# Optimization experiments

Measured on AMD Instinct MI355X. Metric: run time of the kernel, lower is better.

Reference implementation:

```python
import jax, jax.numpy as jnp
import numpy as np

D_MODEL = 2048
N_HEADS = 16
N_KV_HEADS = 4
HEAD_DIM = D_MODEL // N_HEADS  # 128
ROPE_BASE = 10000.0


def _rope_tables(T, head_dim):
    half = head_dim // 2
    theta = 1.0 / (ROPE_BASE ** (jnp.arange(half, dtype=jnp.float32) / half))
    m = jnp.arange(T, dtype=jnp.float32)
    freqs = jnp.outer(m, theta)  # (T, half)
    return jnp.cos(freqs), jnp.sin(freqs)


def _apply_rope(x, cos, sin):
    # x: (B, H, T, hd); rotate first/second halves as pairs
    half = x.shape[-1] // 2
    x1, x2 = x[..., :half], x[..., half:]
    cos = cos[None, None, :, :]
    sin = sin[None, None, :, :]
    return jnp.concatenate([x1 * cos - x2 * sin, x1 * sin + x2 * cos], axis=-1)


def setup_inputs() -> dict:
    key = jax.random.key(0)
    ks = jax.random.split(key, 5)
    B, T = 4, 2048
    x = jax.random.normal(ks[0], (B, T, D_MODEL), dtype=jnp.float32)
    Wq = jax.random.normal(ks[1], (D_MODEL, N_HEADS * HEAD_DIM), dtype=jnp.float32) * 0.02
    Wk = jax.random.normal(ks[2], (D_MODEL, N_KV_HEADS * HEAD_DIM), dtype=jnp.float32) * 0.02
    Wv = jax.random.normal(ks[3], (D_MODEL, N_KV_HEADS * HEAD_DIM), dtype=jnp.float32) * 0.02
    Wo = jax.random.normal(ks[4], (N_HEADS * HEAD_DIM, D_MODEL), dtype=jnp.float32) * (0.02 / np.sqrt(2.0))
    return {"x": x, "Wq": Wq, "Wk": Wk, "Wv": Wv, "Wo": Wo}


def reference(x, Wq, Wk, Wv, Wo):
    B, T, C = x.shape
    groups = N_HEADS // N_KV_HEADS

    # QKV projections
    q = (x @ Wq).reshape(B, T, N_HEADS, HEAD_DIM).transpose(0, 2, 1, 3)      # (B,H,T,hd)
    k = (x @ Wk).reshape(B, T, N_KV_HEADS, HEAD_DIM).transpose(0, 2, 1, 3)   # (B,Hkv,T,hd)
    v = (x @ Wv).reshape(B, T, N_KV_HEADS, HEAD_DIM).transpose(0, 2, 1, 3)

    # RoPE on q and k
    cos, sin = _rope_tables(T, HEAD_DIM)
    q = _apply_rope(q, cos, sin)
    k = _apply_rope(k, cos, sin)

    # GQA: repeat each kv head `groups` times
    k = jnp.repeat(k, groups, axis=1)  # (B,H,T,hd)
    v = jnp.repeat(v, groups, axis=1)

    # Attention scores with ALiBi bias and causal mask
    scale = 1.0 / np.sqrt(HEAD_DIM)
    scores = jnp.einsum('bhqd,bhkd->bhqk', q, k) * scale  # (B,H,T,T)

    pos = jnp.arange(T)
    dist = jnp.minimum(pos[None, :] - pos[:, None], 0).astype(jnp.float32)  # (T,T), <=0
    slopes = 2.0 ** (-8.0 * jnp.arange(1, N_HEADS + 1, dtype=jnp.float32) / N_HEADS)
    alibi = slopes[:, None, None] * dist[None, :, :]  # (H,T,T)
    scores = scores + alibi[None]

    causal = pos[None, :] > pos[:, None]  # True = future = blocked
    scores = jnp.where(causal[None, None], -jnp.inf, scores)

    weights = jax.nn.softmax(scores, axis=-1)
    out = jnp.einsum('bhqk,bhkd->bhqd', weights, v)  # (B,H,T,hd)
    out = out.transpose(0, 2, 1, 3).reshape(B, T, N_HEADS * HEAD_DIM)
    return out @ Wo
```

## Files before the change

kernel.cpp:

```cpp
#include <hip/hip_runtime.h>
#include <hip/hip_bf16.h>
#include <stdint.h>

#define T_SEQ 2048
#define DM    2048
#define NH    16
#define NKVH  4
#define HD    128
#define NBATCH 4
#define BT    (NBATCH * T_SEQ)
#define ATT_SCALE 0.08838834764831845f
#define LOG2E 1.4426950408889634f

typedef __attribute__((ext_vector_type(8))) short bf16x8;
typedef __attribute__((ext_vector_type(4))) float f32x4;
typedef __attribute__((ext_vector_type(16))) float f32x16;
typedef __attribute__((ext_vector_type(8))) unsigned short ushort8;
typedef __attribute__((ext_vector_type(4))) unsigned short ushort4v;

static __device__ __forceinline__ unsigned short f2bf(float f) {
  __hip_bfloat16 h = __float2bfloat16(f);
  return __builtin_bit_cast(unsigned short, h);
}
static __device__ __forceinline__ float bf2f(unsigned short u) {
  unsigned int v = ((unsigned int)u) << 16;
  return __builtin_bit_cast(float, v);
}
static __device__ __forceinline__ unsigned int packbf2(float a, float b) {
  return (unsigned int)f2bf(a) | ((unsigned int)f2bf(b) << 16);
}

#define GLDS16(g, l)                                                        \
  __builtin_amdgcn_global_load_lds(                                         \
      (const __attribute__((address_space(1))) void*)(g),                   \
      (__attribute__((address_space(3))) void*)(l), 16, 0, 0)

__global__ __launch_bounds__(256) void castx_k(const float* __restrict__ x,
                                               unsigned short* __restrict__ xb) {
  int i = (blockIdx.x * 256 + threadIdx.x) * 4;
  float4 v = *(const float4*)&x[i];
  ushort4v o;
  o[0] = f2bf(v.x); o[1] = f2bf(v.y); o[2] = f2bf(v.z); o[3] = f2bf(v.w);
  *(ushort4v*)&xb[i] = o;
}

__global__ __launch_bounds__(256) void transw_k(const float* __restrict__ src,
                                                unsigned short* __restrict__ dst,
                                                int ncols) {
  __shared__ unsigned short t[64][72];
  int n0 = blockIdx.x * 64, r0 = blockIdx.y * 64;
  int tid = threadIdx.x;
  int tx = tid & 15, ty = tid >> 4;
#pragma unroll
  for (int i = 0; i < 4; i++) {
    int r = ty * 4 + i;
    float4 v = *(const float4*)&src[(size_t)(r0 + r) * ncols + n0 + tx * 4];
    t[r][tx * 4 + 0] = f2bf(v.x);
    t[r][tx * 4 + 1] = f2bf(v.y);
    t[r][tx * 4 + 2] = f2bf(v.z);
    t[r][tx * 4 + 3] = f2bf(v.w);
  }
  __syncthreads();
  int nl = tid >> 2, seg = tid & 3;
  ushort8 o0, o1;
#pragma unroll
  for (int j = 0; j < 8; j++) {
    o0[j] = t[seg * 16 + j][nl];
    o1[j] = t[seg * 16 + 8 + j][nl];
  }
  size_t base = (size_t)(n0 + nl) * 2048 + r0 + seg * 16;
  *(ushort8*)&dst[base] = o0;
  *(ushort8*)&dst[base + 8] = o1;
}

template <int EPI>
__global__ __launch_bounds__(256) void gemm_k(const unsigned short* __restrict__ A,
                                              const unsigned short* __restrict__ Bt,
                                              unsigned short* __restrict__ q_out,
                                              unsigned short* __restrict__ k_out,
                                              unsigned short* __restrict__ v_out,
                                              float* __restrict__ f_out) {
  __shared__ unsigned short As[128 * 32];
  __shared__ unsigned short Bs[128 * 32];
  const int tid = threadIdx.x;
  const int lane = tid & 63;
  const int wid = tid >> 6;
  const int wr = wid >> 1, wc = wid & 1;
  const int row0 = blockIdx.x * 128, n00 = blockIdx.y * 128;
  const int lr = lane & 15, lk = (lane >> 4) * 8;
  const int c0 = tid, c1 = tid + 256;

  f32x4 acc[4][4] = {};

  for (int k0 = 0; k0 < 2048; k0 += 32) {
    __syncthreads();
    GLDS16(A + (size_t)(row0 + (c0 >> 2)) * 2048 + k0 + (c0 & 3) * 8, &As[c0 * 8]);
    GLDS16(A + (size_t)(row0 + (c1 >> 2)) * 2048 + k0 + (c1 & 3) * 8, &As[c1 * 8]);
    GLDS16(Bt + (size_t)(n00 + (c0 >> 2)) * 2048 + k0 + (c0 & 3) * 8, &Bs[c0 * 8]);
    GLDS16(Bt + (size_t)(n00 + (c1 >> 2)) * 2048 + k0 + (c1 & 3) * 8, &Bs[c1 * 8]);
    __syncthreads();
    bf16x8 af[4], bfr[4];
#pragma unroll
    for (int mi = 0; mi < 4; mi++)
      af[mi] = *(const bf16x8*)&As[(wr * 64 + mi * 16 + lr) * 32 + lk];
#pragma unroll
    for (int ni = 0; ni < 4; ni++)
      bfr[ni] = *(const bf16x8*)&Bs[(wc * 64 + ni * 16 + lr) * 32 + lk];
#pragma unroll
    for (int mi = 0; mi < 4; mi++)
#pragma unroll
      for (int ni = 0; ni < 4; ni++)
        acc[mi][ni] =
            __builtin_amdgcn_mfma_f32_16x16x32_bf16(af[mi], bfr[ni], acc[mi][ni], 0, 0, 0);
  }

  const int rbase = row0 + wr * 64;
  const int cbase = n00 + wc * 64;
#pragma unroll
  for (int mi = 0; mi < 4; mi++)
#pragma unroll
    for (int ni = 0; ni < 4; ni++)
#pragma unroll
      for (int r = 0; r < 4; r++) {
        int row = rbase + mi * 16 + (lane >> 4) * 4 + r;
        int col = cbase + ni * 16 + lr;
        float v = acc[mi][ni][r];
        if (EPI == 0) {
          if (col < 2048) {
            q_out[(size_t)row * 2048 + col] = f2bf(v);
          } else if (col < 2560) {
            k_out[(size_t)row * 512 + (col - 2048)] = f2bf(v);
          } else {
            int nv = col - 2560;
            int kvh = nv >> 7, d = nv & 127;
            int b = row >> 11, tt = row & 2047;
            v_out[((size_t)(b * NKVH + kvh) * HD + d) * T_SEQ + tt] = f2bf(v);
          }
        } else {
          f_out[(size_t)row * 2048 + col] = v;
        }
      }
}

__global__ __launch_bounds__(256) void rope_k(unsigned short* __restrict__ qb,
                                              unsigned short* __restrict__ kb) {
  int idx = blockIdx.x * 256 + threadIdx.x;
  int i = idx & 63;
  int wi = idx >> 6;
  int hh = wi % (NH + NKVH);
  int bt = wi / (NH + NKVH);
  int t = bt & (T_SEQ - 1);
  unsigned short* p = (hh < NH) ? (qb + (size_t)bt * 2048 + hh * HD)
                                : (kb + (size_t)bt * 512 + (hh - NH) * HD);
  float theta = exp2f(-(float)i * (13.287712379549449f / 64.0f));
  float ang = (float)t * theta;
  float s, c;
  sincosf(ang, &s, &c);
  float x1 = bf2f(p[i]), x2 = bf2f(p[i + 64]);
  p[i] = f2bf(x1 * c - x2 * s);
  p[i + 64] = f2bf(x1 * s + x2 * c);
}

__global__ __launch_bounds__(256) void attn_k(const unsigned short* __restrict__ qb,
                                              const unsigned short* __restrict__ kb,
                                              const unsigned short* __restrict__ vt,
                                              unsigned short* __restrict__ ao) {
  __shared__ __align__(16) unsigned short smem[32768];

  const int bid = blockIdx.x;
  const int s8 = bid & 7;
  const int rest = bid >> 3;
  const int p = rest & 7;
  const int hh = (rest >> 3) & 3;
  const int g = s8 + 8 * (rest >> 5);
  const int b = g >> 2, kvh = g & 3;
  const int h = kvh * 4 + hh;

  const int tid = threadIdx.x;
  const int wid = tid >> 6, lane = tid & 63;
  const int l31 = lane & 31, lh = lane >> 5;
  const float slope2 = exp2f(-0.5f * (float)(h + 1)) * LOG2E;
  const float scale2 = ATT_SCALE * LOG2E;

  const int krow = tid >> 4;
  const int cgk = (tid & 15) ^ (krow & 7);
  const int vrow7 = (tid >> 3) & 7;
  const int cgv = (tid & 7) ^ vrow7;
  const int xr = l31 & 7;

  const unsigned short* khead = kb + (size_t)(b * T_SEQ) * 512 + kvh * 128;
  const unsigned short* vhead = vt + (size_t)(b * NKVH + kvh) * HD * T_SEQ;

  auto stage = [&](int buf, int k0) {
#pragma unroll
    for (int c = 0; c < 4; c++)
      GLDS16(khead + (size_t)(k0 + c * 16 + krow) * 512 + cgk * 8,
             &smem[buf * 8192 + c * 2048 + tid * 8]);
#pragma unroll
    for (int c = 0; c < 4; c++)
      GLDS16(vhead + (size_t)(c * 32 + (tid >> 3)) * T_SEQ + k0 + cgv * 8,
             &smem[16384 + buf * 8192 + c * 2048 + tid * 8]);
  };

  unsigned short (*ot)[32][136] = (unsigned short(*)[32][136])smem;

#pragma unroll 1
  for (int half = 0; half < 2; ++half) {
    const int j = half ? (15 - p) : p;
    const int q0 = j * 128 + wid * 32;
    const int dt32 = j * 4 + wid;
    const int nt = 2 * j + 2;

    const unsigned short* qrow =
        qb + ((size_t)(b * T_SEQ + q0 + l31)) * 2048 + h * HD + lh * 8;
    bf16x8 qf[8];
#pragma unroll
    for (int ds = 0; ds < 8; ds++) qf[ds] = *(const bf16x8*)&qrow[ds * 16];

    f32x16 oacc[4] = {};
    float m2 = -1e30f, l_sum = 0.f;
    const float arow = -slope2 * (float)(q0 + l31);

    __syncthreads();
    stage(0, 64 * (nt - 1));
    __syncthreads();
    int cur = 0;

#pragma unroll 1
    for (int it = 0; it < nt; ++it) {
      const int tt = nt - 1 - it;
      if (it + 1 < nt) stage(cur ^ 1, 64 * (tt - 1));

      const unsigned short* Kb = &smem[cur * 8192];
      const unsigned short* Vb = &smem[16384 + cur * 8192];

#pragma unroll
      for (int ms = 1; ms >= 0; --ms) {
        const int k32 = tt * 2 + ms;
        if (k32 <= dt32) {
          const int k0m = k32 * 32;

          bf16x8 kf[8];
#pragma unroll
          for (int ds = 0; ds < 8; ds++)
            kf[ds] = *(const bf16x8*)&Kb[(ms * 32 + l31) * 128 + ((2 * ds + lh) ^ xr) * 8];

          __builtin_amdgcn_s_setprio(1);
          f32x16 sc = 0.f;
#pragma unroll
          for (int ds = 0; ds < 8; ds++)
            sc = __builtin_amdgcn_mfma_f32_32x32x16_bf16(kf[ds], qf[ds], sc, 0, 0, 0);
          __builtin_amdgcn_s_setprio(0);

          bf16x8 vf[4][2];
#pragma unroll
          for (int dt = 0; dt < 4; dt++)
#pragma unroll
            for (int ks = 0; ks < 2; ks++)
              vf[dt][ks] = *(const bf16x8*)&Vb[(dt * 32 + l31) * 64 +
                                               ((ms * 4 + 2 * ks + lh) ^ xr) * 8];

          float s[16];
          const float ab = fmaf(slope2, (float)k0m, arow);
          const bool diag = (k32 == dt32);
#pragma unroll
          for (int r = 0; r < 16; r++) {
            const int crow = (r & 3) + 8 * (r >> 2) + 4 * lh;
            float v = fmaf(sc[r], scale2, fmaf(slope2, (float)crow, ab));
            if (diag && crow > l31) v = -1e30f;
            s[r] = v;
          }

          float t8[8], t4[4];
#pragma unroll
          for (int i = 0; i < 8; i++) t8[i] = fmaxf(s[i], s[i + 8]);
#pragma unroll
          for (int i = 0; i < 4; i++) t4[i] = fmaxf(t8[i], t8[i + 4]);
          float mx = fmaxf(fmaxf(t4[0], t4[1]), fmaxf(t4[2], t4[3]));
          mx = fmaxf(mx, __shfl_xor(mx, 32));

          if (__any(mx > m2 + 8.f)) {
            const float mnew = fmaxf(m2, mx);
            const float corr = exp2f(m2 - mnew);
            l_sum *= corr;
#pragma unroll
            for (int dt = 0; dt < 4; dt++) oacc[dt] *= corr;
            m2 = mnew;
          }

          float pr[16];
#pragma unroll
          for (int r = 0; r < 16; r++) pr[r] = exp2f(s[r] - m2);

          float a8[8], a4[4];
#pragma unroll
          for (int i = 0; i < 8; i++) a8[i] = pr[i] + pr[i + 8];
#pragma unroll
          for (int i = 0; i < 4; i++) a4[i] = a8[i] + a8[i + 4];
          float rs = (a4[0] + a4[1]) + (a4[2] + a4[3]);
          rs += __shfl_xor(rs, 32);
          l_sum += rs;

          unsigned int w[8];
#pragma unroll
          for (int i = 0; i < 8; i++) w[i] = packbf2(pr[2 * i], pr[2 * i + 1]);
          const unsigned int ta = __shfl_xor(lh ? w[0] : w[2], 32);
          const unsigned int tb = __shfl_xor(lh ? w[1] : w[3], 32);
          const unsigned int tc = __shfl_xor(lh ? w[4] : w[6], 32);
          const unsigned int td = __shfl_xor(lh ? w[5] : w[7], 32);
          union U4 { unsigned int u[4]; bf16x8 v; } f0, f1;
          f0.u[0] = lh ? ta : w[0];
          f0.u[1] = lh ? tb : w[1];
          f0.u[2] = lh ? w[2] : ta;
          f0.u[3] = lh ? w[3] : tb;
          f1.u[0] = lh ? tc : w[4];
          f1.u[1] = lh ? td : w[5];
          f1.u[2] = lh ? w[6] : tc;
          f1.u[3] = lh ? w[7] : td;

          __builtin_amdgcn_s_setprio(1);
#pragma unroll
          for (int dt = 0; dt < 4; dt++) {
            oacc[dt] =
                __builtin_amdgcn_mfma_f32_32x32x16_bf16(vf[dt][0], f0.v, oacc[dt], 0, 0, 0);
            oacc[dt] =
                __builtin_amdgcn_mfma_f32_32x32x16_bf16(vf[dt][1], f1.v, oacc[dt], 0, 0, 0);
          }
          __builtin_amdgcn_s_setprio(0);
        }
      }

      __syncthreads();
      cur ^= 1;
    }

    const float inv = 1.0f / l_sum;
#pragma unroll
    for (int dt = 0; dt < 4; dt++)
#pragma unroll
      for (int rg = 0; rg < 4; rg++) {
        ushort4v o;
#pragma unroll
        for (int jj = 0; jj < 4; jj++) o[jj] = f2bf(oacc[dt][rg * 4 + jj] * inv);
        *(ushort4v*)&ot[wid][l31][dt * 32 + rg * 8 + lh * 4] = o;
      }
    __syncthreads();
    const int rrow = lane >> 4, chunk = lane & 15;
#pragma unroll
    for (int ps = 0; ps < 8; ps++) {
      const int row = ps * 4 + rrow;
      ushort8 v = *(const ushort8*)&ot[wid][row][chunk * 8];
      *(ushort8*)&ao[((size_t)(b * T_SEQ + q0 + row)) * 2048 + h * HD + chunk * 8] = v;
    }
  }
}

extern "C" void kernel_launch(void* const* d_in, const int* in_sizes, int n_in,
                              void* d_out, int out_size, void* d_ws, size_t ws_size,
                              hipStream_t stream) {
  const float* x = (const float*)d_in[0];
  const float* Wq = (const float*)d_in[1];
  const float* Wk = (const float*)d_in[2];
  const float* Wv = (const float*)d_in[3];
  const float* Wo = (const float*)d_in[4];

  char* w = (char*)d_ws;
  unsigned short* xb = (unsigned short*)w;
  unsigned short* wqt = (unsigned short*)(w + 33554432);
  unsigned short* qb = (unsigned short*)(w + 33554432 + 12582912);
  unsigned short* kb = (unsigned short*)(w + 33554432 + 12582912 + 33554432);
  unsigned short* vtb = (unsigned short*)(w + 33554432 + 12582912 + 33554432 + 8388608);

  castx_k<<<16384, 256, 0, stream>>>(x, xb);
  transw_k<<<dim3(32, 32), 256, 0, stream>>>(Wq, wqt, 2048);
  transw_k<<<dim3(8, 32), 256, 0, stream>>>(Wk, wqt + (size_t)2048 * 2048, 512);
  transw_k<<<dim3(8, 32), 256, 0, stream>>>(Wv, wqt + (size_t)2560 * 2048, 512);
  gemm_k<0><<<dim3(64, 24), 256, 0, stream>>>(xb, wqt, qb, kb, vtb, nullptr);
  rope_k<<<40960, 256, 0, stream>>>(qb, kb);
  transw_k<<<dim3(32, 32), 256, 0, stream>>>(Wo, wqt, 2048);
  attn_k<<<512, 256, 0, stream>>>(qb, kb, vtb, xb);
  gemm_k<1><<<dim3(64, 16), 256, 0, stream>>>(xb, wqt, nullptr, nullptr, nullptr,
                                              (float*)d_out);
}
```

Baseline: 471.1 us.

## Restructure attention into one q-tile per block with triple-buffered 32-key tiles

The attention kernel stops pairing two causal q-tiles per block and launches one block per q-tile (1024 blocks), scheduling the heaviest tiles first. K/V staging moves from double-buffered 64-key tiles to triple-buffered 32-key tiles, using explicit vmcnt waits and a single barrier per step, and launch_bounds(256,3) with smaller shared memory aims for more resident blocks. Exponentials are computed speculatively before the rescale check, and the row-sum shuffle is deferred to the end. The aim is better overlap and occupancy; the cost is finer-grained steps with more barriers, and possible register pressure from the occupancy hint.

```diff
diff --git a/kernel.cpp b/kernel.cpp
--- a/kernel.cpp
+++ b/kernel.cpp
@@ -161,197 +161,190 @@
   p[i + 64] = f2bf(x1 * s + x2 * c);
 }
 
-__global__ __launch_bounds__(256) void attn_k(const unsigned short* __restrict__ qb,
-                                              const unsigned short* __restrict__ kb,
-                                              const unsigned short* __restrict__ vt,
-                                              unsigned short* __restrict__ ao) {
-  __shared__ __align__(16) unsigned short smem[32768];
+__global__ __launch_bounds__(256, 3) void attn_k(const unsigned short* __restrict__ qb,
+                                                 const unsigned short* __restrict__ kb,
+                                                 const unsigned short* __restrict__ vt,
+                                                 unsigned short* __restrict__ ao) {
+  __shared__ __align__(16) unsigned short smem[24576];
 
   const int bid = blockIdx.x;
-  const int s8 = bid & 7;
-  const int rest = bid >> 3;
-  const int p = rest & 7;
-  const int hh = (rest >> 3) & 3;
-  const int g = s8 + 8 * (rest >> 5);
+  const int j = 15 - (bid >> 6);
+  const int g = (bid & 7) | (((bid >> 3) & 1) << 3);
+  const int hh = (bid >> 4) & 3;
   const int b = g >> 2, kvh = g & 3;
   const int h = kvh * 4 + hh;
 
   const int tid = threadIdx.x;
   const int wid = tid >> 6, lane = tid & 63;
   const int l31 = lane & 31, lh = lane >> 5;
+  const int xr = l31 & 7;
   const float slope2 = exp2f(-0.5f * (float)(h + 1)) * LOG2E;
   const float scale2 = ATT_SCALE * LOG2E;
 
+  const int q0 = j * 128 + wid * 32;
+  const int dt_w = j * 4 + wid;
+  const int nt = j * 4 + 4;
+
   const int krow = tid >> 4;
   const int cgk = (tid & 15) ^ (krow & 7);
-  const int vrow7 = (tid >> 3) & 7;
-  const int cgv = (tid & 7) ^ vrow7;
-  const int xr = l31 & 7;
+  const int vr = tid >> 3;
+  const int cgv = (tid & 7) ^ (vr & 7);
 
   const unsigned short* khead = kb + (size_t)(b * T_SEQ) * 512 + kvh * 128;
   const unsigned short* vhead = vt + (size_t)(b * NKVH + kvh) * HD * T_SEQ;
 
-  auto stage = [&](int buf, int k0) {
-#pragma unroll
-    for (int c = 0; c < 4; c++)
-      GLDS16(khead + (size_t)(k0 + c * 16 + krow) * 512 + cgk * 8,
-             &smem[buf * 8192 + c * 2048 + tid * 8]);
-#pragma unroll
-    for (int c = 0; c < 4; c++)
-      GLDS16(vhead + (size_t)(c * 32 + (tid >> 3)) * T_SEQ + k0 + cgv * 8,
-             &smem[16384 + buf * 8192 + c * 2048 + tid * 8]);
+  auto stage = [&](int slot, int tile) {
+    const int k0 = tile * 32;
+    unsigned short* base = &smem[slot * 8192];
+    GLDS16(khead + (size_t)(k0 + krow) * 512 + cgk * 8, base + tid * 8);
+    GLDS16(khead + (size_t)(k0 + 16 + krow) * 512 + cgk * 8, base + 2048 + tid * 8);
+    GLDS16(vhead + (size_t)(((cgv >> 2) << 6) + vr) * T_SEQ + k0 + (cgv & 3) * 8,
+           base + 4096 + tid * 8);
+    GLDS16(vhead + (size_t)(((cgv >> 2) << 6) + 32 + vr) * T_SEQ + k0 + (cgv & 3) * 8,
+           base + 6144 + tid * 8);
   };
 
   unsigned short (*ot)[32][136] = (unsigned short(*)[32][136])smem;
 
+  const unsigned short* qrow =
+      qb + ((size_t)(b * T_SEQ + q0 + l31)) * 2048 + h * HD + lh * 8;
+  bf16x8 qf[8];
+#pragma unroll
+  for (int ds = 0; ds < 8; ds++) qf[ds] = *(const bf16x8*)&qrow[ds * 16];
+
+  f32x16 oacc[4] = {};
+  float m2 = -1e30f, l_half = 0.f;
+  const float arow = -slope2 * (float)(q0 + l31);
+
+  stage(0, nt - 1);
+  stage(1, nt - 2);
+
 #pragma unroll 1
-  for (int half = 0; half < 2; ++half) {
-    const int j = half ? (15 - p) : p;
-    const int q0 = j * 128 + wid * 32;
-    const int dt32 = j * 4 + wid;
-    const int nt = 2 * j + 2;
-
-    const unsigned short* qrow =
-        qb + ((size_t)(b * T_SEQ + q0 + l31)) * 2048 + h * HD + lh * 8;
-    bf16x8 qf[8];
-#pragma unroll
-    for (int ds = 0; ds < 8; ds++) qf[ds] = *(const bf16x8*)&qrow[ds * 16];
-
-    f32x16 oacc[4] = {};
-    float m2 = -1e30f, l_sum = 0.f;
-    const float arow = -slope2 * (float)(q0 + l31);
-
-    __syncthreads();
-    stage(0, 64 * (nt - 1));
-    __syncthreads();
-    int cur = 0;
-
-#pragma unroll 1
-    for (int it = 0; it < nt; ++it) {
-      const int tt = nt - 1 - it;
-      if (it + 1 < nt) stage(cur ^ 1, 64 * (tt - 1));
-
-      const unsigned short* Kb = &smem[cur * 8192];
-      const unsigned short* Vb = &smem[16384 + cur * 8192];
-
-#pragma unroll
-      for (int ms = 1; ms >= 0; --ms) {
-        const int k32 = tt * 2 + ms;
-        if (k32 <= dt32) {
-          const int k0m = k32 * 32;
-
-          bf16x8 kf[8];
-#pragma unroll
-          for (int ds = 0; ds < 8; ds++)
-            kf[ds] = *(const bf16x8*)&Kb[(ms * 32 + l31) * 128 + ((2 * ds + lh) ^ xr) * 8];
-
-          __builtin_amdgcn_s_setprio(1);
-          f32x16 sc = 0.f;
-#pragma unroll
-          for (int ds = 0; ds < 8; ds++)
-            sc = __builtin_amdgcn_mfma_f32_32x32x16_bf16(kf[ds], qf[ds], sc, 0, 0, 0);
-          __builtin_amdgcn_s_setprio(0);
-
-          bf16x8 vf[4][2];
-#pragma unroll
-          for (int dt = 0; dt < 4; dt++)
-#pragma unroll
-            for (int ks = 0; ks < 2; ks++)
-              vf[dt][ks] = *(const bf16x8*)&Vb[(dt * 32 + l31) * 64 +
-                                               ((ms * 4 + 2 * ks + lh) ^ xr) * 8];
-
-          float s[16];
-          const float ab = fmaf(slope2, (float)k0m, arow);
-          const bool diag = (k32 == dt32);
-#pragma unroll
-          for (int r = 0; r < 16; r++) {
-            const int crow = (r & 3) + 8 * (r >> 2) + 4 * lh;
-            float v = fmaf(sc[r], scale2, fmaf(slope2, (float)crow, ab));
-            if (diag && crow > l31) v = -1e30f;
-            s[r] = v;
-          }
-
-          float t8[8], t4[4];
-#pragma unroll
-          for (int i = 0; i < 8; i++) t8[i] = fmaxf(s[i], s[i + 8]);
-#pragma unroll
-          for (int i = 0; i < 4; i++) t4[i] = fmaxf(t8[i], t8[i + 4]);
-          float mx = fmaxf(fmaxf(t4[0], t4[1]), fmaxf(t4[2], t4[3]));
-          mx = fmaxf(mx, __shfl_xor(mx, 32));
-
-          if (__any(mx > m2 + 8.f)) {
-            const float mnew = fmaxf(m2, mx);
-            const float corr = exp2f(m2 - mnew);
-            l_sum *= corr;
-#pragma unroll
-            for (int dt = 0; dt < 4; dt++) oacc[dt] *= corr;
-            m2 = mnew;
-          }
-
-          float pr[16];
-#pragma unroll
-          for (int r = 0; r < 16; r++) pr[r] = exp2f(s[r] - m2);
-
-          float a8[8], a4[4];
-#pragma unroll
-          for (int i = 0; i < 8; i++) a8[i] = pr[i] + pr[i + 8];
-#pragma unroll
-          for (int i = 0; i < 4; i++) a4[i] = a8[i] + a8[i + 4];
-          float rs = (a4[0] + a4[1]) + (a4[2] + a4[3]);
-          rs += __shfl_xor(rs, 32);
-          l_sum += rs;
-
-          unsigned int w[8];
-#pragma unroll
-          for (int i = 0; i < 8; i++) w[i] = packbf2(pr[2 * i], pr[2 * i + 1]);
-          const unsigned int ta = __shfl_xor(lh ? w[0] : w[2], 32);
-          const unsigned int tb = __shfl_xor(lh ? w[1] : w[3], 32);
-          const unsigned int tc = __shfl_xor(lh ? w[4] : w[6], 32);
-          const unsigned int td = __shfl_xor(lh ? w[5] : w[7], 32);
-          union U4 { unsigned int u[4]; bf16x8 v; } f0, f1;
-          f0.u[0] = lh ? ta : w[0];
-          f0.u[1] = lh ? tb : w[1];
-          f0.u[2] = lh ? w[2] : ta;
-          f0.u[3] = lh ? w[3] : tb;
-          f1.u[0] = lh ? tc : w[4];
-          f1.u[1] = lh ? td : w[5];
-          f1.u[2] = lh ? w[6] : tc;
-          f1.u[3] = lh ? w[7] : td;
-
-          __builtin_amdgcn_s_setprio(1);
-#pragma unroll
-          for (int dt = 0; dt < 4; dt++) {
-            oacc[dt] =
-                __builtin_amdgcn_mfma_f32_32x32x16_bf16(vf[dt][0], f0.v, oacc[dt], 0, 0, 0);
-            oacc[dt] =
-                __builtin_amdgcn_mfma_f32_32x32x16_bf16(vf[dt][1], f1.v, oacc[dt], 0, 0, 0);
-          }
-          __builtin_amdgcn_s_setprio(0);
-        }
+  for (int it = 0; it < nt; ++it) {
+    const int tt = nt - 1 - it;
+    if (it == nt - 1) {
+      asm volatile("s_waitcnt vmcnt(0)" ::: "memory");
+    } else {
+      asm volatile("s_waitcnt vmcnt(4)" ::: "memory");
+    }
+    asm volatile("s_barrier" ::: "memory");
+    if (tt >= 2) stage((it + 2) % 3, tt - 2);
+
+    if (tt <= dt_w) {
+      const int slot = it % 3;
+      const unsigned short* Kb = &smem[slot * 8192];
+      const unsigned short* Vb = &smem[slot * 8192 + 4096];
+      const int k0 = tt * 32;
+
+      bf16x8 kf[8];
+#pragma unroll
+      for (int ds = 0; ds < 8; ds++)
+        kf[ds] = *(const bf16x8*)&Kb[l31 * 128 + ((2 * ds + lh) ^ xr) * 8];
+
+      __builtin_amdgcn_s_setprio(1);
+      f32x16 sc = 0.f;
+#pragma unroll
+      for (int ds = 0; ds < 8; ds++)
+        sc = __builtin_amdgcn_mfma_f32_32x32x16_bf16(kf[ds], qf[ds], sc, 0, 0, 0);
+      __builtin_amdgcn_s_setprio(0);
+
+      bf16x8 vf[4][2];
+#pragma unroll
+      for (int dt = 0; dt < 4; dt++)
+#pragma unroll
+        for (int ks = 0; ks < 2; ks++)
+          vf[dt][ks] = *(const bf16x8*)&Vb[((dt & 1) * 32 + l31) * 64 +
+                                           (((dt >> 1) * 4 + 2 * ks + lh) ^ xr) * 8];
+
+      float s[16];
+      const float ab = fmaf(slope2, (float)k0, arow);
+      const bool diag = (tt == dt_w);
+#pragma unroll
+      for (int r = 0; r < 16; r++) {
+        const int crow = (r & 3) + 8 * (r >> 2) + 4 * lh;
+        float v = fmaf(sc[r], scale2, fmaf(slope2, (float)crow, ab));
+        if (diag && crow > l31) v = -1e30f;
+        s[r] = v;
       }
 
-      __syncthreads();
-      cur ^= 1;
+      float t8[8], t4[4];
+#pragma unroll
+      for (int i = 0; i < 8; i++) t8[i] = fmaxf(s[i], s[i + 8]);
+#pragma unroll
+      for (int i = 0; i < 4; i++) t4[i] = fmaxf(t8[i], t8[i + 4]);
+      float mx = fmaxf(fmaxf(t4[0], t4[1]), fmaxf(t4[2], t4[3]));
+
+      float pr[16];
+#pragma unroll
+      for (int r = 0; r < 16; r++) pr[r] = exp2f(s[r] - m2);
+
+      mx = fmaxf(mx, __shfl_xor(mx, 32));
+      if (__any(mx > m2 + 8.f)) {
+        const float mnew = fmaxf(m2, mx);
+        const float corr = exp2f(m2 - mnew);
+        l_half *= corr;
+#pragma unroll
+        for (int dt = 0; dt < 4; dt++) oacc[dt] *= corr;
+#pragma unroll
+        for (int r = 0; r < 16; r++) pr[r] = exp2f(s[r] - mnew);
+        m2 = mnew;
+      }
+
+      float a8[8], a4[4];
+#pragma unroll
+      for (int i = 0; i < 8; i++) a8[i] = pr[i] + pr[i + 8];
+#pragma unroll
+      for (int i = 0; i < 4; i++) a4[i] = a8[i] + a8[i + 4];
+      l_half += (a4[0] + a4[1]) + (a4[2] + a4[3]);
+
+      unsigned int w[8];
+#pragma unroll
+      for (int i = 0; i < 8; i++) w[i] = packbf2(pr[2 * i], pr[2 * i + 1]);
+      const unsigned int ta = __shfl_xor(lh ? w[0] : w[2], 32);
+      const unsigned int tb = __shfl_xor(lh ? w[1] : w[3], 32);
+      const unsigned int tc = __shfl_xor(lh ? w[4] : w[6], 32);
+      const unsigned int td = __shfl_xor(lh ? w[5] : w[7], 32);
+      union U4 { unsigned int u[4]; bf16x8 v; } f0, f1;
+      f0.u[0] = lh ? ta : w[0];
+      f0.u[1] = lh ? tb : w[1];
+      f0.u[2] = lh ? w[2] : ta;
+      f0.u[3] = lh ? w[3] : tb;
+      f1.u[0] = lh ? tc : w[4];
+      f1.u[1] = lh ? td : w[5];
+      f1.u[2] = lh ? w[6] : tc;
+      f1.u[3] = lh ? w[7] : td;
+
+      __builtin_amdgcn_s_setprio(1);
+#pragma unroll
+      for (int dt = 0; dt < 4; dt++) {
+        oacc[dt] =
+            __builtin_amdgcn_mfma_f32_32x32x16_bf16(vf[dt][0], f0.v, oacc[dt], 0, 0, 0);
+        oacc[dt] =
+            __builtin_amdgcn_mfma_f32_32x32x16_bf16(vf[dt][1], f1.v, oacc[dt], 0, 0, 0);
+      }
+      __builtin_amdgcn_s_setprio(0);
     }
-
-    const float inv = 1.0f / l_sum;
-#pragma unroll
-    for (int dt = 0; dt < 4; dt++)
-#pragma unroll
-      for (int rg = 0; rg < 4; rg++) {
-        ushort4v o;
-#pragma unroll
-        for (int jj = 0; jj < 4; jj++) o[jj] = f2bf(oacc[dt][rg * 4 + jj] * inv);
-        *(ushort4v*)&ot[wid][l31][dt * 32 + rg * 8 + lh * 4] = o;
-      }
-    __syncthreads();
-    const int rrow = lane >> 4, chunk = lane & 15;
-#pragma unroll
-    for (int ps = 0; ps < 8; ps++) {
-      const int row = ps * 4 + rrow;
-      ushort8 v = *(const ushort8*)&ot[wid][row][chunk * 8];
-      *(ushort8*)&ao[((size_t)(b * T_SEQ + q0 + row)) * 2048 + h * HD + chunk * 8] = v;
+  }
+
+  const float l_tot = l_half + __shfl_xor(l_half, 32);
+  const float inv = 1.0f / l_tot;
+  __syncthreads();
+#pragma unroll
+  for (int dt = 0; dt < 4; dt++)
+#pragma unroll
+    for (int rg = 0; rg < 4; rg++) {
+      ushort4v o;
+#pragma unroll
+      for (int jj = 0; jj < 4; jj++) o[jj] = f2bf(oacc[dt][rg * 4 + jj] * inv);
+      *(ushort4v*)&ot[wid][l31][dt * 32 + rg * 8 + lh * 4] = o;
     }
+  __syncthreads();
+  const int rrow = lane >> 4, chunk = lane & 15;
+#pragma unroll
+  for (int ps = 0; ps < 8; ps++) {
+    const int row = ps * 4 + rrow;
+    ushort8 v = *(const ushort8*)&ot[wid][row][chunk * 8];
+    *(ushort8*)&ao[((size_t)(b * T_SEQ + q0 + row)) * 2048 + h * HD + chunk * 8] = v;
   }
 }
 
@@ -378,7 +371,7 @@
   gemm_k<0><<<dim3(64, 24), 256, 0, stream>>>(xb, wqt, qb, kb, vtb, nullptr);
   rope_k<<<40960, 256, 0, stream>>>(qb, kb);
   transw_k<<<dim3(32, 32), 256, 0, stream>>>(Wo, wqt, 2048);
-  attn_k<<<512, 256, 0, stream>>>(qb, kb, vtb, xb);
+  attn_k<<<1024, 256, 0, stream>>>(qb, kb, vtb, xb);
   gemm_k<1><<<dim3(64, 16), 256, 0, stream>>>(xb, wqt, nullptr, nullptr, nullptr,
                                               (float*)d_out);
 }
```

Result: slower. 576.7 us (+22.4%).
